# Kernel tuning notes

Measured on AMD Instinct MI355X. Metric: run time of the kernel, lower is better.

## Reference

```python
import jax, jax.numpy as jnp
import numpy as np

NUM_HEADS = 4
EPS = 1e-12  # torch F.normalize eps


def _l2norm(t):
    # normalize along last axis, matching torch.nn.functional.normalize
    n = jnp.sqrt(jnp.sum(t * t, axis=-1, keepdims=True))
    return t / jnp.maximum(n, EPS)


def setup_inputs() -> dict:
    key = jax.random.key(0)
    k1, k2 = jax.random.split(key)
    B, N, C = 4, 8192, 768
    x = jax.random.normal(k1, (B, N, C), dtype=jnp.float32)
    W_qkvv = jax.random.normal(k2, (3 * C, C), dtype=jnp.float32) * (C ** -0.5)
    temperature = jnp.ones((NUM_HEADS, 1, 1), dtype=jnp.float32)
    return {"x": x, "W_qkvv": W_qkvv, "temperature": temperature}


def reference(x, W_qkvv, temperature):
    B, N, C = x.shape
    H = NUM_HEADS
    D = C // H
    # qkvv projection: [B,N,3C] -> [3,B,H,N,D]
    qkvv = (x @ W_qkvv.T).reshape(B, N, 3, H, D).transpose(2, 0, 3, 1, 4)
    q, k, v = qkvv[0], qkvv[1], qkvv[2]        # each [B,H,N,D]
    q = jnp.swapaxes(q, -2, -1)                # [B,H,D,N]
    k = jnp.swapaxes(k, -2, -1)                # [B,H,D,N]
    v = jnp.swapaxes(v, -2, -1)                # [B,H,D,N]
    q = _l2norm(q)
    k = _l2norm(k)
    # channel attention scores: [B,H,D,D], temperature broadcast per head
    attn = jnp.einsum('bhdn,bhen->bhde', q, k) * temperature[None]
    attn = jax.nn.softmax(attn, axis=-1)
    # dropout is identity in eval mode
    x_CA = jnp.einsum('bhde,bhen->bhdn', attn, v)   # [B,H,D,N]
    out = x_CA.transpose(0, 3, 1, 2).reshape(B, N, C)
    return out
```

## Files before the change

kernel.cpp:

```cpp
#include <hip/hip_runtime.h>
#include <hip/hip_bf16.h>
#include <cstddef>
#include <cstdint>

#define B_   4
#define N_   8192
#define C_   768
#define H_   4
#define D_   192
#define CQ_  2304
#define M_   32768

typedef __attribute__((ext_vector_type(8))) short short8_t;
typedef __attribute__((ext_vector_type(4))) float f32x4;

typedef const __attribute__((address_space(1))) uint gq_uint;
typedef __attribute__((address_space(3))) uint lds_uint;

__device__ inline ushort f2bf(float f){
  uint u = __float_as_uint(f);
  u += 0x7FFFu + ((u >> 16) & 1u);
  return (ushort)(u >> 16);
}
__device__ inline float bf2f(ushort u){ return __uint_as_float(((uint)u) << 16); }

__global__ __launch_bounds__(256) void cvt_bf16(const float* __restrict__ src,
                                                ushort* __restrict__ dst, int n4){
  int i = blockIdx.x * 256 + threadIdx.x;
  if (i < n4){
    float4 v = ((const float4*)src)[i];
    ushort4 o;
    o.x = f2bf(v.x); o.y = f2bf(v.y); o.z = f2bf(v.z); o.w = f2bf(v.w);
    ((ushort4*)dst)[i] = o;
  }
}

__global__ __launch_bounds__(256) void gemm_qkvv(const ushort* __restrict__ A,
                                                 const ushort* __restrict__ W,
                                                 ushort* __restrict__ Cq,
                                                 float* __restrict__ norm2){
  __shared__ __align__(16) ushort As[128 * 32];
  __shared__ __align__(16) ushort Bs[128 * 32];
  const int t = threadIdx.x;
  const int m0 = blockIdx.y * 128;
  const int n0 = blockIdx.x * 128;
  const int w  = t >> 6, lane = t & 63;
  const int wr = w >> 1, wc = w & 1;
  const int lr = lane & 15, lg = lane >> 4;

  f32x4 acc[4][4];
  #pragma unroll
  for (int i = 0; i < 4; ++i)
    #pragma unroll
    for (int j = 0; j < 4; ++j)
      acc[i][j] = (f32x4){0.f, 0.f, 0.f, 0.f};

  const int srow = lane >> 2;
  const int scol = (lane & 3) * 8;

  for (int kt = 0; kt < 24; ++kt){
    const int k0 = kt * 32;
    __syncthreads();
    #pragma unroll
    for (int i = 0; i < 2; ++i){
      const int c = w * 2 + i;
      const int row = c * 16 + srow;
      __builtin_amdgcn_global_load_lds(
          (gq_uint*)(const void*)(A + (size_t)(m0 + row) * 768 + k0 + scol),
          (lds_uint*)(void*)&As[c * 512], 16, 0, 0);
      __builtin_amdgcn_global_load_lds(
          (gq_uint*)(const void*)(W + (size_t)(n0 + row) * 768 + k0 + scol),
          (lds_uint*)(void*)&Bs[c * 512], 16, 0, 0);
    }
    __syncthreads();
    short8_t af[4], bf[4];
    #pragma unroll
    for (int f = 0; f < 4; ++f)
      af[f] = *(const short8_t*)(&As[(wr*64 + f*16 + lr) * 32 + lg*8]);
    #pragma unroll
    for (int f = 0; f < 4; ++f)
      bf[f] = *(const short8_t*)(&Bs[(wc*64 + f*16 + lr) * 32 + lg*8]);
    #pragma unroll
    for (int i = 0; i < 4; ++i)
      #pragma unroll
      for (int j = 0; j < 4; ++j)
        acc[i][j] = __builtin_amdgcn_mfma_f32_16x16x32_bf16(af[i], bf[j], acc[i][j], 0, 0, 0);
  }

  #pragma unroll
  for (int i = 0; i < 4; ++i)
    #pragma unroll
    for (int j = 0; j < 4; ++j)
      #pragma unroll
      for (int r = 0; r < 4; ++r){
        int m = m0 + wr*64 + i*16 + lg*4 + r;
        int c = n0 + wc*64 + j*16 + lr;
        Cq[(size_t)m * CQ_ + c] = f2bf(acc[i][j][r]);
      }

  if (n0 < 1536){
    const int b = m0 >> 13;
    #pragma unroll
    for (int j = 0; j < 4; ++j){
      float s = 0.f;
      #pragma unroll
      for (int i = 0; i < 4; ++i)
        #pragma unroll
        for (int r = 0; r < 4; ++r)
          s = fmaf(acc[i][j][r], acc[i][j][r], s);
      s += __shfl_xor(s, 16);
      s += __shfl_xor(s, 32);
      if (lg == 0)
        atomicAdd(&norm2[b * 1536 + n0 + wc*64 + j*16 + lr], s);
    }
  }
}

__global__ __launch_bounds__(256) void gram_mfma(const ushort* __restrict__ Qk,
                                                 float* __restrict__ Sp){
  const int kc = blockIdx.x;
  const int bh = blockIdx.y;
  const int eh = blockIdx.z;
  const int b = bh >> 2, h = bh & 3;
  __shared__ __align__(16) ushort qs[32][194];
  __shared__ __align__(16) ushort ks[32][98];
  const int t = threadIdx.x;
  const int w = t >> 6, lane = t & 63;
  const int wd = w >> 1, we = w & 1;
  const int lr = lane & 15, lg = lane >> 4;

  f32x4 acc[6][3];
  #pragma unroll
  for (int i = 0; i < 6; ++i)
    #pragma unroll
    for (int j = 0; j < 3; ++j)
      acc[i][j] = (f32x4){0.f, 0.f, 0.f, 0.f};

  const uint* qb = (const uint*)Qk + ((size_t)b * N_ * CQ_ + h * 192) / 2;
  const uint* kb = (const uint*)Qk + ((size_t)b * N_ * CQ_ + 768 + h * 192 + eh * 96) / 2;

  for (int it = 0; it < 16; ++it){
    const int n0 = kc * 512 + it * 32;
    __syncthreads();
    #pragma unroll
    for (int u = 0; u < 3; ++u){
      int g = u * 256 + t;
      int row = g / 24, c4 = g % 24;
      uint4 v = ((const uint4*)(qb + (size_t)(n0 + row) * 1152))[c4];
      uint* dst = (uint*)&qs[row][8 * c4];
      dst[0] = v.x; dst[1] = v.y; dst[2] = v.z; dst[3] = v.w;
    }
    #pragma unroll
    for (int u = 0; u < 3; ++u){
      int g = u * 256 + t;
      int row = g / 24, c2 = g % 24;
      uint2 v = ((const uint2*)(kb + (size_t)(n0 + row) * 1152))[c2];
      uint* dst = (uint*)&ks[row][4 * c2];
      dst[0] = v.x; dst[1] = v.y;
    }
    __syncthreads();
    union { uint u[4]; short8_t v; } af[6], bf[3];
    #pragma unroll
    for (int i = 0; i < 6; ++i){
      int d = wd * 96 + i * 16 + lr;
      #pragma unroll
      for (int p = 0; p < 4; ++p)
        af[i].u[p] = (uint)qs[lg*8 + 2*p][d] | ((uint)qs[lg*8 + 2*p + 1][d] << 16);
    }
    #pragma unroll
    for (int j = 0; j < 3; ++j){
      int e = we * 48 + j * 16 + lr;
      #pragma unroll
      for (int p = 0; p < 4; ++p)
        bf[j].u[p] = (uint)ks[lg*8 + 2*p][e] | ((uint)ks[lg*8 + 2*p + 1][e] << 16);
    }
    #pragma unroll
    for (int i = 0; i < 6; ++i)
      #pragma unroll
      for (int j = 0; j < 3; ++j)
        acc[i][j] = __builtin_amdgcn_mfma_f32_16x16x32_bf16(af[i].v, bf[j].v, acc[i][j], 0, 0, 0);
  }
  float* base = Sp + (size_t)(kc * 16 + bh) * 192 * 192;
  #pragma unroll
  for (int i = 0; i < 6; ++i)
    #pragma unroll
    for (int j = 0; j < 3; ++j)
      #pragma unroll
      for (int r = 0; r < 4; ++r){
        int d = wd * 96 + i * 16 + lg * 4 + r;
        int e = eh * 96 + we * 48 + j * 16 + lr;
        base[(size_t)d * 192 + e] = acc[i][j][r];
      }
}

__global__ __launch_bounds__(256) void softmax_k(const float* __restrict__ Sp,
                                                 const float* __restrict__ norm2,
                                                 const float* __restrict__ temp,
                                                 ushort* __restrict__ attn){
  const int wid  = blockIdx.x * 4 + (threadIdx.x >> 6);
  const int lane = threadIdx.x & 63;
  const int bh = wid / 192, d = wid % 192;
  const int b = bh >> 2, h = bh & 3;
  const float nq = sqrtf(norm2[b*1536 + h*192 + d]);
  const float sc = temp[h] / fmaxf(nq, 1e-12f);
  const float* Sr = Sp + ((size_t)bh * 192 + d) * 192;
  float l[3];
  #pragma unroll
  for (int u = 0; u < 3; ++u){
    int e = lane + u * 64;
    float s = 0.f;
    #pragma unroll
    for (int kc = 0; kc < 16; ++kc)
      s += Sr[(size_t)kc * (16*192*192) + e];
    float nk = sqrtf(norm2[b*1536 + 768 + h*192 + e]);
    l[u] = s * sc / fmaxf(nk, 1e-12f);
  }
  float m = fmaxf(l[0], fmaxf(l[1], l[2]));
  #pragma unroll
  for (int off = 32; off; off >>= 1) m = fmaxf(m, __shfl_xor(m, off));
  float p[3], s = 0.f;
  #pragma unroll
  for (int u = 0; u < 3; ++u){ p[u] = expf(l[u] - m); s += p[u]; }
  #pragma unroll
  for (int off = 32; off; off >>= 1) s += __shfl_xor(s, off);
  float inv = 1.f / s;
  ushort* ar = attn + ((size_t)bh * 192 + d) * 192;
  #pragma unroll
  for (int u = 0; u < 3; ++u) ar[lane + u*64] = f2bf(p[u] * inv);
}

__global__ __launch_bounds__(256) void out_gemm(const ushort* __restrict__ Q,
                                                const ushort* __restrict__ attn,
                                                float* __restrict__ out){
  const int bh = blockIdx.y;
  const int b = bh >> 2, h = bh & 3;
  const int n0 = blockIdx.x * 128;
  const int t = threadIdx.x, w = t >> 6, lane = t & 63;
  const int wn = w & 1, wd = w >> 1;
  const int lr = lane & 15, lg = lane >> 4;
  f32x4 acc[4][6];
  #pragma unroll
  for (int i = 0; i < 4; ++i)
    #pragma unroll
    for (int j = 0; j < 6; ++j)
      acc[i][j] = (f32x4){0.f, 0.f, 0.f, 0.f};

  const ushort* Vbase = Q + 1536 + h * 192;
  const ushort* Abase = attn + (size_t)bh * 192 * 192;

  #pragma unroll
  for (int kk = 0; kk < 6; ++kk){
    const int e = kk * 32 + lg * 8;
    short8_t av[4], bv[6];
    #pragma unroll
    for (int f = 0; f < 4; ++f){
      int n = n0 + wn*64 + f*16 + lr;
      av[f] = *(const short8_t*)(Vbase + (size_t)(b*N_ + n) * CQ_ + e);
    }
    #pragma unroll
    for (int f = 0; f < 6; ++f){
      int d = wd*96 + f*16 + lr;
      bv[f] = *(const short8_t*)(Abase + d * 192 + e);
    }
    #pragma unroll
    for (int i = 0; i < 4; ++i)
      #pragma unroll
      for (int j = 0; j < 6; ++j)
        acc[i][j] = __builtin_amdgcn_mfma_f32_16x16x32_bf16(av[i], bv[j], acc[i][j], 0, 0, 0);
  }
  #pragma unroll
  for (int i = 0; i < 4; ++i)
    #pragma unroll
    for (int j = 0; j < 6; ++j)
      #pragma unroll
      for (int r = 0; r < 4; ++r){
        int n = n0 + wn*64 + i*16 + lg*4 + r;
        int c = h*192 + wd*96 + j*16 + lr;
        out[(size_t)(b*N_ + n) * 768 + c] = acc[i][j][r];
      }
}

extern "C" void kernel_launch(void* const* d_in, const int* in_sizes, int n_in,
                              void* d_out, int out_size, void* d_ws, size_t ws_size,
                              hipStream_t stream){
  const float* x    = (const float*)d_in[0];
  const float* Wq   = (const float*)d_in[1];
  const float* temp = (const float*)d_in[2];
  float* out = (float*)d_out;
  char* ws = (char*)d_ws;

  ushort* xb    = (ushort*)(ws + 0);
  float*  S_part= (float*)(ws + 0);
  ushort* attn  = (ushort*)(ws + 37748736);
  ushort* Wb    = (ushort*)(ws + 50331648);
  ushort* qkvv  = (ushort*)(ws + 53870592);
  float*  norm2 = (float*)(ws + 204865536);

  hipMemsetAsync(norm2, 0, 24576, stream);

  cvt_bf16<<<6291456/256, 256, 0, stream>>>(x,  xb, 6291456);
  cvt_bf16<<<442368/256,  256, 0, stream>>>(Wq, Wb, 442368);

  gemm_qkvv<<<dim3(18, 256), 256, 0, stream>>>(xb, Wb, qkvv, norm2);

  gram_mfma<<<dim3(16, 16, 2), 256, 0, stream>>>(qkvv, S_part);
  softmax_k<<<768, 256, 0, stream>>>(S_part, norm2, temp, attn);
  out_gemm<<<dim3(64, 16), 256, 0, stream>>>(qkvv, attn, out);
}
```

Before: 287.3 us.

## Rewrite QKV GEMM with 256x256 tiles, double-buffered swizzled LDS, and XCD-aware block mapping

The QKV projection GEMM moves from a 128x128 tile with a single LDS buffer and two barriers per 32-wide k-step to a 256x256 tile with 512 threads. It uses a 64-wide k-step and double-buffered dynamic LDS (128 KB), so the next stage's global-to-LDS loads overlap the MFMAs. LDS columns are XOR-swizzled to avoid bank conflicts, setprio raises wave priority around the MFMA bursts, and blocks are remapped so consecutive IDs spread across XCDs for L2 locality. The larger tile raises arithmetic intensity and cuts redundant loads, in exchange for more register pressure and fewer resident blocks per CU.

After: 240.0 us. 16.5% less time.

```diff
diff --git a/kernel.cpp b/kernel.cpp
--- a/kernel.cpp
+++ b/kernel.cpp
@@ -35,83 +35,126 @@
   }
 }
 
-__global__ __launch_bounds__(256) void gemm_qkvv(const ushort* __restrict__ A,
-                                                 const ushort* __restrict__ W,
-                                                 ushort* __restrict__ Cq,
-                                                 float* __restrict__ norm2){
-  __shared__ __align__(16) ushort As[128 * 32];
-  __shared__ __align__(16) ushort Bs[128 * 32];
+__global__ __launch_bounds__(512, 2) void gemm_qkvv(const ushort* __restrict__ A,
+                                                    const ushort* __restrict__ W,
+                                                    ushort* __restrict__ Cq,
+                                                    float* __restrict__ norm2){
+  extern __shared__ ushort lds[];
   const int t = threadIdx.x;
-  const int m0 = blockIdx.y * 128;
-  const int n0 = blockIdx.x * 128;
-  const int w  = t >> 6, lane = t & 63;
-  const int wr = w >> 1, wc = w & 1;
+  const int bid = blockIdx.x;
+  const int wg  = (bid & 7) * 144 + (bid >> 3);
+  const int by = wg / 9, bx = wg % 9;
+  const int m0 = by * 256, n0 = bx * 256;
+  const int wid = t >> 6, lane = t & 63;
+  const int wm = wid >> 2, wn = wid & 3;
   const int lr = lane & 15, lg = lane >> 4;
-
-  f32x4 acc[4][4];
-  #pragma unroll
-  for (int i = 0; i < 4; ++i)
+  const int srow  = lane >> 3;
+  const int sslot = (lane & 7) ^ srow;
+
+  f32x4 acc[8][4];
+  #pragma unroll
+  for (int i = 0; i < 8; ++i)
     #pragma unroll
     for (int j = 0; j < 4; ++j)
       acc[i][j] = (f32x4){0.f, 0.f, 0.f, 0.f};
 
-  const int srow = lane >> 2;
-  const int scol = (lane & 3) * 8;
-
-  for (int kt = 0; kt < 24; ++kt){
-    const int k0 = kt * 32;
-    __syncthreads();
-    #pragma unroll
-    for (int i = 0; i < 2; ++i){
-      const int c = w * 2 + i;
-      const int row = c * 16 + srow;
-      __builtin_amdgcn_global_load_lds(
-          (gq_uint*)(const void*)(A + (size_t)(m0 + row) * 768 + k0 + scol),
-          (lds_uint*)(void*)&As[c * 512], 16, 0, 0);
-      __builtin_amdgcn_global_load_lds(
-          (gq_uint*)(const void*)(W + (size_t)(n0 + row) * 768 + k0 + scol),
-          (lds_uint*)(void*)&Bs[c * 512], 16, 0, 0);
-    }
-    __syncthreads();
-    short8_t af[4], bf[4];
-    #pragma unroll
-    for (int f = 0; f < 4; ++f)
-      af[f] = *(const short8_t*)(&As[(wr*64 + f*16 + lr) * 32 + lg*8]);
-    #pragma unroll
-    for (int f = 0; f < 4; ++f)
-      bf[f] = *(const short8_t*)(&Bs[(wc*64 + f*16 + lr) * 32 + lg*8]);
-    #pragma unroll
-    for (int i = 0; i < 4; ++i)
-      #pragma unroll
-      for (int j = 0; j < 4; ++j)
-        acc[i][j] = __builtin_amdgcn_mfma_f32_16x16x32_bf16(af[i], bf[j], acc[i][j], 0, 0, 0);
-  }
-
-  #pragma unroll
-  for (int i = 0; i < 4; ++i)
-    #pragma unroll
-    for (int j = 0; j < 4; ++j)
+  #define STAGE(KT, CUR)                                                          \
+    do {                                                                          \
+      const int k0_ = (KT) * 64;                                                  \
+      ushort* bA_ = lds + (CUR) * 32768;                                          \
+      ushort* bB_ = bA_ + 16384;                                                  \
+      _Pragma("unroll")                                                           \
+      for (int i_ = 0; i_ < 4; ++i_){                                             \
+        const int r_ = i_ * 64 + wid * 8;                                         \
+        __builtin_amdgcn_global_load_lds(                                         \
+            (gq_uint*)(const void*)(A + (size_t)(m0 + r_ + srow) * 768 + k0_ + sslot * 8), \
+            (lds_uint*)(void*)(bA_ + r_ * 64), 16, 0, 0);                         \
+        __builtin_amdgcn_global_load_lds(                                         \
+            (gq_uint*)(const void*)(W + (size_t)(n0 + r_ + srow) * 768 + k0_ + sslot * 8), \
+            (lds_uint*)(void*)(bB_ + r_ * 64), 16, 0, 0);                         \
+      }                                                                           \
+    } while (0)
+
+  STAGE(0, 0);
+  STAGE(1, 1);
+  asm volatile("s_waitcnt vmcnt(8)" ::: "memory");
+  __builtin_amdgcn_s_barrier();
+  __builtin_amdgcn_sched_barrier(0);
+
+  for (int kt = 0; kt < 12; ++kt){
+    const int cur = kt & 1;
+    const ushort* bA = lds + cur * 32768;
+    const ushort* bB = bA + 16384;
+
+    short8_t af[2][8], bf[2][4];
+    #pragma unroll
+    for (int kk = 0; kk < 2; ++kk){
+      const int sl = ((kk * 4 + lg) ^ (lr & 7)) * 8;
+      #pragma unroll
+      for (int fm = 0; fm < 8; ++fm)
+        af[kk][fm] = *(const short8_t*)(bA + (wm * 128 + fm * 16 + lr) * 64 + sl);
+      #pragma unroll
+      for (int fn = 0; fn < 4; ++fn)
+        bf[kk][fn] = *(const short8_t*)(bB + (wn * 64 + fn * 16 + lr) * 64 + sl);
+    }
+
+    __builtin_amdgcn_s_setprio(1);
+    #pragma unroll
+    for (int fm = 0; fm < 8; ++fm)
+      #pragma unroll
+      for (int fn = 0; fn < 4; ++fn)
+        acc[fm][fn] = __builtin_amdgcn_mfma_f32_16x16x32_bf16(af[0][fm], bf[0][fn], acc[fm][fn], 0, 0, 0);
+    __builtin_amdgcn_s_setprio(0);
+
+    asm volatile("s_waitcnt lgkmcnt(0)" ::: "memory");
+    __builtin_amdgcn_sched_barrier(0);
+    __builtin_amdgcn_s_barrier();
+    __builtin_amdgcn_sched_barrier(0);
+
+    if (kt + 2 < 12) STAGE(kt + 2, cur);
+
+    __builtin_amdgcn_s_setprio(1);
+    #pragma unroll
+    for (int fm = 0; fm < 8; ++fm)
+      #pragma unroll
+      for (int fn = 0; fn < 4; ++fn)
+        acc[fm][fn] = __builtin_amdgcn_mfma_f32_16x16x32_bf16(af[1][fm], bf[1][fn], acc[fm][fn], 0, 0, 0);
+    __builtin_amdgcn_s_setprio(0);
+
+    if (kt < 11){
+      if (kt + 2 < 12) asm volatile("s_waitcnt vmcnt(8)" ::: "memory");
+      else             asm volatile("s_waitcnt vmcnt(0)" ::: "memory");
+      __builtin_amdgcn_s_barrier();
+      __builtin_amdgcn_sched_barrier(0);
+    }
+  }
+  #undef STAGE
+
+  #pragma unroll
+  for (int fm = 0; fm < 8; ++fm)
+    #pragma unroll
+    for (int fn = 0; fn < 4; ++fn)
       #pragma unroll
       for (int r = 0; r < 4; ++r){
-        int m = m0 + wr*64 + i*16 + lg*4 + r;
-        int c = n0 + wc*64 + j*16 + lr;
-        Cq[(size_t)m * CQ_ + c] = f2bf(acc[i][j][r]);
+        int m = m0 + wm * 128 + fm * 16 + lg * 4 + r;
+        int c = n0 + wn * 64 + fn * 16 + lr;
+        Cq[(size_t)m * CQ_ + c] = f2bf(acc[fm][fn][r]);
       }
 
-  if (n0 < 1536){
+  if (bx < 6){
     const int b = m0 >> 13;
     #pragma unroll
-    for (int j = 0; j < 4; ++j){
+    for (int fn = 0; fn < 4; ++fn){
       float s = 0.f;
       #pragma unroll
-      for (int i = 0; i < 4; ++i)
+      for (int fm = 0; fm < 8; ++fm)
         #pragma unroll
         for (int r = 0; r < 4; ++r)
-          s = fmaf(acc[i][j][r], acc[i][j][r], s);
+          s = fmaf(acc[fm][fn][r], acc[fm][fn][r], s);
       s += __shfl_xor(s, 16);
       s += __shfl_xor(s, 32);
       if (lg == 0)
-        atomicAdd(&norm2[b * 1536 + n0 + wc*64 + j*16 + lr], s);
+        atomicAdd(&norm2[b * 1536 + n0 + wn * 64 + fn * 16 + lr], s);
     }
   }
 }
@@ -296,12 +339,16 @@
   ushort* qkvv  = (ushort*)(ws + 53870592);
   float*  norm2 = (float*)(ws + 204865536);
 
+  static_assert(sizeof(ushort) == 2, "");
+  hipFuncSetAttribute((const void*)gemm_qkvv,
+                      hipFuncAttributeMaxDynamicSharedMemorySize, 131072);
+
   hipMemsetAsync(norm2, 0, 24576, stream);
 
   cvt_bf16<<<6291456/256, 256, 0, stream>>>(x,  xb, 6291456);
   cvt_bf16<<<442368/256,  256, 0, stream>>>(Wq, Wb, 442368);
 
-  gemm_qkvv<<<dim3(18, 256), 256, 0, stream>>>(xb, Wb, qkvv, norm2);
+  gemm_qkvv<<<1152, 512, 131072, stream>>>(xb, Wb, qkvv, norm2);
 
   gram_mfma<<<dim3(16, 16, 2), 256, 0, stream>>>(qkvv, S_part);
   softmax_k<<<768, 256, 0, stream>>>(S_part, norm2, temp, attn);
```
